# Performance work log

Hardware: AMD Instinct MI355X
Metric: run time of the kernel (lower is better)

Reference implementation:

```python
import jax, jax.numpy as jnp
import numpy as np

B, S, H = 2, 2048, 4096
NH, HD = 32, 128          # num attention heads, head dim (kv_channels)
KVH = 2                   # multi_query_group_num (KV heads)
ROT = HD // 2             # 64 rotary dims -> rope cache last-2 dim = 32
QKV = NH * HD + 2 * KVH * HD  # 4608


def apply_rope(x, rope):
    # x: [b, nh, s, hd]; rope: [b, s, ROT//2, 2]
    b, nh, s, hd = x.shape
    x_rot, x_pass = x[..., :ROT], x[..., ROT:]
    xs = x_rot.reshape(b, nh, s, ROT // 2, 2)
    rc = rope[:, :s].reshape(b, 1, s, ROT // 2, 2)
    out = jnp.stack([
        xs[..., 0] * rc[..., 0] - xs[..., 1] * rc[..., 1],
        xs[..., 1] * rc[..., 0] + xs[..., 0] * rc[..., 1],
    ], axis=-1).reshape(b, nh, s, ROT)
    return jnp.concatenate([out, x_pass], axis=-1)


def setup_inputs() -> dict:
    key = jax.random.key(0)
    ks = jax.random.split(key, 6)
    hidden_states = jax.random.normal(ks[0], (B, S, H), dtype=jnp.float32)
    rotary_pos_emb = jax.random.normal(ks[1], (B, S, ROT // 2, 2), dtype=jnp.float32)
    # causal mask: True = masked (strict upper triangle), matching module's ~tril
    causal = jnp.triu(jnp.ones((S, S), dtype=jnp.bool_), k=1)
    attention_mask = jnp.broadcast_to(causal[None, None], (B, 1, S, S))
    W_qkv = jax.random.normal(ks[2], (QKV, H), dtype=jnp.float32) * (1.0 / np.sqrt(H))
    b_qkv = jax.random.normal(ks[3], (QKV,), dtype=jnp.float32) * 0.02
    W_dense = jax.random.normal(ks[4], (H, NH * HD), dtype=jnp.float32) * (1.0 / np.sqrt(NH * HD))
    return {"hidden_states": hidden_states, "rotary_pos_emb": rotary_pos_emb,
            "attention_mask": attention_mask, "W_qkv": W_qkv, "b_qkv": b_qkv,
            "W_dense": W_dense}


def reference(hidden_states, rotary_pos_emb, attention_mask, W_qkv, b_qkv, W_dense):
    b, s, _ = hidden_states.shape
    mixed = hidden_states @ W_qkv.T + b_qkv  # [b, s, QKV]
    q, k, v = jnp.split(mixed, [NH * HD, NH * HD + KVH * HD], axis=-1)
    q = q.reshape(b, s, NH, HD).transpose(0, 2, 1, 3)   # [b, NH, s, hd]
    k = k.reshape(b, s, KVH, HD).transpose(0, 2, 1, 3)  # [b, KVH, s, hd]
    v = v.reshape(b, s, KVH, HD).transpose(0, 2, 1, 3)
    q = apply_rope(q, rotary_pos_emb)
    k = apply_rope(k, rotary_pos_emb)
    # GQA expand KV heads to NH
    rep = NH // KVH
    k = jnp.repeat(k, rep, axis=1)
    v = jnp.repeat(v, rep, axis=1)
    scale = 1.0 / np.sqrt(HD)
    scores = jnp.einsum('bhqd,bhkd->bhqk', q, k).astype(jnp.float32) * scale
    scores = jnp.where(attention_mask, -jnp.inf, scores)
    probs = jax.nn.softmax(scores, axis=-1).astype(v.dtype)
    ctx = jnp.einsum('bhqk,bhkd->bhqd', probs, v)       # [b, NH, s, hd]
    ctx = ctx.transpose(0, 2, 1, 3).reshape(b, s, NH * HD)
    return ctx @ W_dense.T
```

## Files before the change

kernel.cpp:

```cpp
#include <hip/hip_runtime.h>
#include <hip/hip_bf16.h>
#include <stdint.h>

#define Bb 2
#define Ss 2048
#define Hh 4096
#define NHh 32
#define HDd 128
#define KVHh 2

typedef __attribute__((ext_vector_type(8))) short bf16x8;
typedef __attribute__((ext_vector_type(4))) float f32x4;
typedef __attribute__((ext_vector_type(16))) float f32x16;
typedef __attribute__((ext_vector_type(4))) unsigned int u32x4;
typedef unsigned short u16;
typedef unsigned int u32;
typedef unsigned long long u64;

__device__ __forceinline__ u16 f2b(float f) {
  union { float f; u32 u; } v; v.f = f;
  u32 r = v.u + 0x7fffu + ((v.u >> 16) & 1u);
  return (u16)(r >> 16);
}
__device__ __forceinline__ float b2f(u16 h) {
  union { u32 u; float f; } v; v.u = ((u32)h) << 16;
  return v.f;
}

__device__ __forceinline__ u32 cvtpk(float lo, float hi_) {
  u32 r;
  asm("v_cvt_pk_bf16_f32 %0, %1, %2" : "=v"(r) : "v"(lo), "v"(hi_));
  return r;
}
__device__ __forceinline__ void plswap(u32& x, u32& y) {
  asm volatile("v_permlane32_swap_b32 %0, %1" : "+v"(x), "+v"(y));
}

__device__ __forceinline__ void gload_lds16(const u16* g, u16* l) {
  __builtin_amdgcn_global_load_lds(
      (const __attribute__((address_space(1))) u32*)(uintptr_t)g,
      (__attribute__((address_space(3))) u32*)(u32)(uintptr_t)l,
      16, 0, 0);
}

__global__ void cvt2_k(const float* __restrict__ a, u16* __restrict__ oa,
                       const float* __restrict__ b, u16* __restrict__ ob) {
  int i = blockIdx.x * blockDim.x + threadIdx.x;
  const float* src;
  u16* dst;
  int off;
  if (i < 4194304) { src = a; dst = oa; off = i; }
  else { src = b; dst = ob; off = i - 4194304; }
  int idx = off * 4;
  float4 v = *(const float4*)&src[idx];
  u64 pack = (u64)f2b(v.x) | ((u64)f2b(v.y) << 16) |
             ((u64)f2b(v.z) << 32) | ((u64)f2b(v.w) << 48);
  *(u64*)&dst[idx] = pack;
}

__global__ void cvtW_k(const float* __restrict__ in, u16* __restrict__ out) {
  int i = blockIdx.x * blockDim.x + threadIdx.x;
  int idx = i * 4;
  float4 v = *(const float4*)&in[idx];
  u64 pack = (u64)f2b(v.x) | ((u64)f2b(v.y) << 16) |
             ((u64)f2b(v.z) << 32) | ((u64)f2b(v.w) << 48);
  *(u64*)&out[idx] = pack;
}

__global__ void rope_k(u16* __restrict__ X, const float* __restrict__ rope, int nheads) {
  int i = blockIdx.x * blockDim.x + threadIdx.x;
  int p = i & 31;
  int s = (i >> 5) & (Ss - 1);
  int bh = i >> 16;
  if (bh >= Bb * nheads) return;
  int b = bh / nheads;
  size_t base = ((size_t)bh * Ss + s) * HDd + p * 2;
  u32 x01 = *(u32*)&X[base];
  float x0 = b2f((u16)(x01 & 0xffff));
  float x1 = b2f((u16)(x01 >> 16));
  float2 rc = *(const float2*)&rope[(((size_t)b * Ss + s) * 32 + p) * 2];
  float o0 = x0 * rc.x - x1 * rc.y;
  float o1 = x1 * rc.x + x0 * rc.y;
  u32 o = (u32)f2b(o0) | ((u32)f2b(o1) << 16);
  *(u32*)&X[base] = o;
}

template <int KK>
__device__ __forceinline__ void stage_tileA(const u16* __restrict__ gbase, u16* dst, int tid) {
#pragma unroll
  for (int li = 0; li < 2; ++li) {
    int t16 = li * 512 + tid;
    int rt = t16 >> 2, ct = t16 & 3;
    int cg = ct ^ ((rt >> 1) & 3);
    gload_lds16(gbase + (size_t)rt * KK + cg * 8, dst + t16 * 8);
  }
}
template <int KK>
__device__ __forceinline__ void stage_tileB(const u16* __restrict__ gbase, u16* dst, int tid) {
  int t16 = tid;
  int rt = t16 >> 2, ct = t16 & 3;
  int cg = ct ^ ((rt >> 1) & 3);
  gload_lds16(gbase + (size_t)rt * KK + cg * 8, dst + t16 * 8);
}

__device__ __forceinline__ bf16x8 frag128(const u16* buf, int row, int lk) {
  int ch = lk ^ ((row >> 1) & 3);
  return *(const bf16x8*)&buf[row * 32 + ch * 8];
}

template <int NN, int KK, int COLG>
__global__ __launch_bounds__(512, 4) void gemm_qkv(
    const u16* __restrict__ A, const u16* __restrict__ Bm,
    const float* __restrict__ bias,
    u16* __restrict__ Qb, u16* __restrict__ Kb, u16* __restrict__ Vb) {
  __shared__ u16 As[2][8192];
  __shared__ u16 Bs[2][4096];
  const int tid = threadIdx.x;
  const int wave = tid >> 6;
  const int lane = tid & 63;
  const int lr = lane & 15;
  const int lk = lane >> 4;
  const int wr = wave >> 1;
  const int wc = wave & 1;
  const int bid = blockIdx.x;
  const int xcd = bid & 7;
  const int local = bid >> 3;
  const int rlr = local / COLG;
  const int rlc = local - rlr * COLG;
  const int m0 = ((xcd >> 2) * 8 + rlr) * 256;
  const int n0 = ((xcd & 3) * COLG + rlc) * 128;
  const int NT = KK / 32;

  f32x4 acc[4][4];
#pragma unroll
  for (int i = 0; i < 4; ++i)
#pragma unroll
    for (int j = 0; j < 4; ++j) acc[i][j] = (f32x4){0.f, 0.f, 0.f, 0.f};

  const u16* Ab = A + (size_t)m0 * KK;
  const u16* Bw = Bm + (size_t)n0 * KK;

  stage_tileA<KK>(Ab, &As[0][0], tid);
  stage_tileB<KK>(Bw, &Bs[0][0], tid);
  asm volatile("s_waitcnt vmcnt(0)");
  __syncthreads();

  int cur = 0;
  for (int t = 0; t < NT; ++t) {
    if (t + 1 < NT) {
      stage_tileA<KK>(Ab + (t + 1) * 32, &As[cur ^ 1][0], tid);
      stage_tileB<KK>(Bw + (t + 1) * 32, &Bs[cur ^ 1][0], tid);
      asm volatile("s_waitcnt vmcnt(3)");
    } else {
      asm volatile("s_waitcnt vmcnt(0)");
    }
    __builtin_amdgcn_s_barrier();
    __builtin_amdgcn_sched_barrier(0);

    bf16x8 af[4], bf[4];
#pragma unroll
    for (int mi = 0; mi < 4; ++mi)
      af[mi] = frag128(&As[cur][0], wr * 64 + mi * 16 + lr, lk);
#pragma unroll
    for (int ni = 0; ni < 4; ++ni)
      bf[ni] = frag128(&Bs[cur][0], wc * 64 + ni * 16 + lr, lk);
    asm volatile("s_waitcnt lgkmcnt(0)");
    __builtin_amdgcn_sched_barrier(0);
    __builtin_amdgcn_s_setprio(1);
#pragma unroll
    for (int mi = 0; mi < 4; ++mi)
#pragma unroll
      for (int ni = 0; ni < 4; ++ni)
        acc[mi][ni] = __builtin_amdgcn_mfma_f32_16x16x32_bf16(af[mi], bf[ni], acc[mi][ni], 0, 0, 0);
    __builtin_amdgcn_s_setprio(0);
    __builtin_amdgcn_s_barrier();
    cur ^= 1;
  }

#pragma unroll
  for (int ni = 0; ni < 4; ++ni) {
    int n = n0 + wc * 64 + ni * 16 + lr;
    float bv = bias[n];
#pragma unroll
    for (int mi = 0; mi < 4; ++mi) {
      int mb = m0 + wr * 64 + mi * 16 + lk * 4;
#pragma unroll
      for (int j = 0; j < 4; ++j) {
        int m = mb + j;
        int bb = m >> 11;
        int ss = m & 2047;
        u16 hv = f2b(acc[mi][ni][j] + bv);
        if (n < 4096) {
          Qb[(((size_t)bb * NHh + (n >> 7)) * Ss + ss) * HDd + (n & 127)] = hv;
        } else if (n < 4352) {
          int idx2 = n - 4096;
          Kb[(((size_t)bb * KVHh + (idx2 >> 7)) * Ss + ss) * HDd + (idx2 & 127)] = hv;
        } else {
          int idx2 = n - 4352;
          Vb[(((size_t)bb * KVHh + (idx2 >> 7)) * Ss + ss) * HDd + (idx2 & 127)] = hv;
        }
      }
    }
  }
}

__global__ __launch_bounds__(512, 2) void gemm_dense8p(
    const u16* __restrict__ A, const u16* __restrict__ Bm,
    float* __restrict__ Cout) {
  __shared__ u16 Ar[3][256 * 64];
  __shared__ u16 Bd[2][128 * 64];
  const int tid = threadIdx.x;
  const int wave = tid >> 6;
  const int lane = tid & 63;
  const int lr = lane & 15;
  const int lk = lane >> 4;
  const int wr = wave >> 1;
  const int wc = wave & 1;
  const int bid = blockIdx.x;
  const int xcd = bid & 7;
  const int local = bid >> 3;
  const int m0 = ((xcd >> 2) * 8 + (local >> 3)) * 256;
  const int n0 = ((xcd & 3) * 8 + (local & 7)) * 128;

  f32x4 acc[4][4];
#pragma unroll
  for (int i = 0; i < 4; ++i)
#pragma unroll
    for (int j = 0; j < 4; ++j) acc[i][j] = (f32x4){0.f, 0.f, 0.f, 0.f};

  auto STAGE_A = [&](int j, int ring) {
    if (j >= 64) return;
#pragma unroll
    for (int li = 0; li < 4; ++li) {
      int t16 = li * 512 + tid;
      int row = t16 >> 3, c = t16 & 7;
      int cs = c ^ (row & 7);
      gload_lds16(A + (size_t)(m0 + row) * 4096 + j * 64 + cs * 8,
                  &Ar[ring][0] + t16 * 8);
    }
  };
  auto STAGE_B = [&](int j) {
    if (j >= 64) return;
#pragma unroll
    for (int li = 0; li < 2; ++li) {
      int t16 = li * 512 + tid;
      int row = t16 >> 3, c = t16 & 7;
      int cs = c ^ (row & 7);
      gload_lds16(Bm + (size_t)(n0 + row) * 4096 + j * 64 + cs * 8,
                  &Bd[j & 1][0] + t16 * 8);
    }
  };

  STAGE_A(0, 0); STAGE_B(0);
  STAGE_A(1, 1); STAGE_B(1);
  asm volatile("s_waitcnt vmcnt(6)");
  __builtin_amdgcn_s_barrier();
  __builtin_amdgcn_sched_barrier(0);

  int ra = 0;
  int ra2 = 2;
  for (int kt = 0; kt < 64; ++kt) {
    const u16* Acur = &Ar[ra][0];
    const u16* Bt = &Bd[kt & 1][0];
    auto rdA = [&](int r, int kk) {
      int ch = (kk * 4 + lk) ^ (r & 7);
      return *(const bf16x8*)&Acur[r * 64 + ch * 8];
    };
    auto rdB = [&](int r, int kk) {
      int ch = (kk * 4 + lk) ^ (r & 7);
      return *(const bf16x8*)&Bt[r * 64 + ch * 8];
    };

    bf16x8 bfr[4][2], af[2][2];
#pragma unroll
    for (int ni = 0; ni < 4; ++ni)
#pragma unroll
      for (int kk = 0; kk < 2; ++kk)
        bfr[ni][kk] = rdB(wc * 64 + ni * 16 + lr, kk);
#pragma unroll
    for (int i = 0; i < 2; ++i)
#pragma unroll
      for (int kk = 0; kk < 2; ++kk)
        af[i][kk] = rdA(wr * 64 + i * 16 + lr, kk);
    STAGE_A(kt + 2, ra2);
    __builtin_amdgcn_s_barrier();
    asm volatile("s_waitcnt lgkmcnt(0)");
    __builtin_amdgcn_sched_barrier(0);
    __builtin_amdgcn_s_setprio(1);
#pragma unroll
    for (int i = 0; i < 2; ++i)
#pragma unroll
      for (int ni = 0; ni < 4; ++ni)
#pragma unroll
        for (int kk = 0; kk < 2; ++kk)
          acc[i][ni] = __builtin_amdgcn_mfma_f32_16x16x32_bf16(af[i][kk], bfr[ni][kk], acc[i][ni], 0, 0, 0);
    __builtin_amdgcn_s_setprio(0);
    __builtin_amdgcn_s_barrier();

#pragma unroll
    for (int i = 0; i < 2; ++i)
#pragma unroll
      for (int kk = 0; kk < 2; ++kk)
        af[i][kk] = rdA(wr * 64 + (2 + i) * 16 + lr, kk);
    STAGE_B(kt + 2);
    __builtin_amdgcn_s_barrier();
    asm volatile("s_waitcnt lgkmcnt(0)");
    __builtin_amdgcn_sched_barrier(0);
    __builtin_amdgcn_s_setprio(1);
#pragma unroll
    for (int i = 0; i < 2; ++i)
#pragma unroll
      for (int ni = 0; ni < 4; ++ni)
#pragma unroll
        for (int kk = 0; kk < 2; ++kk)
          acc[2 + i][ni] = __builtin_amdgcn_mfma_f32_16x16x32_bf16(af[i][kk], bfr[ni][kk], acc[2 + i][ni], 0, 0, 0);
    __builtin_amdgcn_s_setprio(0);
    if (kt < 62) {
      asm volatile("s_waitcnt vmcnt(6)");
    } else {
      asm volatile("s_waitcnt vmcnt(0)");
    }
    __builtin_amdgcn_s_barrier();
    __builtin_amdgcn_sched_barrier(0);

    ra = (ra == 2) ? 0 : ra + 1;
    ra2 = (ra2 == 2) ? 0 : ra2 + 1;
  }

#pragma unroll
  for (int mi = 0; mi < 4; ++mi)
#pragma unroll
    for (int ni = 0; ni < 4; ++ni) {
      int col = n0 + wc * 64 + ni * 16 + lr;
      int rowb = m0 + wr * 64 + mi * 16 + lk * 4;
#pragma unroll
      for (int j = 0; j < 4; ++j)
        Cout[(size_t)(rowb + j) * 4096 + col] = acc[mi][ni][j];
    }
}

__global__ __launch_bounds__(512, 2) void attn_k(
    const u16* __restrict__ Qb, const u16* __restrict__ Kb,
    const u16* __restrict__ Vb, const float* __restrict__ rope,
    u16* __restrict__ Ctx) {
  __shared__ u16 Kt[2][64 * 128];
  __shared__ u16 Vt[2][128 * 64];
  const int tid = threadIdx.x;
  const int w = tid >> 6;
  const int lane = tid & 63;
  const int l31 = lane & 31;
  const int hi = lane >> 5;
  const int h = blockIdx.y, b = blockIdx.z;
  const int hkv = h >> 4;
  const u16* Qp = Qb + ((size_t)(b * NHh + h)) * Ss * HDd;
  const u16* Kp = Kb + ((size_t)(b * KVHh + hkv)) * Ss * HDd;
  const u16* Vp = Vb + ((size_t)(b * KVHh + hkv)) * Ss * HDd;

  const float scale = 0.08838834764831845f;
  const float L2E = 1.4426950408889634f;

  for (int hp = 0; hp < 2; ++hp) {
    const int qt = hp == 0 ? (7 - (int)blockIdx.x) : (int)blockIdx.x;
    const int qs = qt * 256;
    const int qw = qs + w * 32;
    const int qrow = qw + l31;
    const int nt = qs / 64 + 4;

    bf16x8 qf[8];
#pragma unroll
    for (int ds = 0; ds < 8; ++ds)
      qf[ds] = *(const bf16x8*)&Qp[(size_t)qrow * HDd + ds * 16 + hi * 8];
#pragma unroll
    for (int ds = 0; ds < 4; ++ds) {
      bf16x8 q = qf[ds];
      bf16x8 o;
#pragma unroll
      for (int i = 0; i < 4; ++i) {
        int p = ds * 8 + hi * 4 + i;
        float2 rc = *(const float2*)&rope[(((size_t)b * Ss + qrow) * 32 + p) * 2];
        float x0 = b2f((u16)q[2 * i]), x1 = b2f((u16)q[2 * i + 1]);
        o[2 * i] = (short)f2b(x0 * rc.x - x1 * rc.y);
        o[2 * i + 1] = (short)f2b(x1 * rc.x + x0 * rc.y);
      }
      qf[ds] = o;
    }

    f32x16 accO[4];
#pragma unroll
    for (int i = 0; i < 4; ++i)
#pragma unroll
      for (int r = 0; r < 16; ++r) accO[i][r] = 0.f;
    float m_r = -3.0e38f, l_r = 0.f;

    {
#pragma unroll
      for (int i = 0; i < 2; ++i) {
        int slot = w * 2 + i;
        int r = slot * 4 + (lane >> 4);
        int p = lane & 15;
        int gc = (p & 8) | ((p ^ r) & 7);
        gload_lds16(Kp + (size_t)r * HDd + gc * 8, &Kt[0][slot * 512]);
      }
      bf16x8 v0 = *(const bf16x8*)&Vp[(size_t)lane * HDd + w * 16];
      bf16x8 v1 = *(const bf16x8*)&Vp[(size_t)lane * HDd + w * 16 + 8];
      u32x4 sv = __builtin_bit_cast(u32x4, (lane & 1) ? v0 : v1);
      u32x4 rv;
      rv.x = __shfl_xor(sv.x, 1); rv.y = __shfl_xor(sv.y, 1);
      rv.z = __shfl_xor(sv.z, 1); rv.w = __shfl_xor(sv.w, 1);
      bf16x8 recv = __builtin_bit_cast(bf16x8, rv);
      int kvp = lane >> 1;
#pragma unroll
      for (int i = 0; i < 8; ++i) {
        int d = w * 16 + (lane & 1) * 8 + i;
        u16 lo = (lane & 1) ? (u16)recv[i] : (u16)v0[i];
        u16 hb = (lane & 1) ? (u16)v1[i] : (u16)recv[i];
        u32 val = (u32)lo | ((u32)hb << 16);
        int cp = (kvp >> 2) ^ (d & 7);
        *(u32*)&Vt[0][d * 64 + cp * 8 + (kvp & 3) * 2] = val;
      }
    }
    __syncthreads();

    for (int t = 0; t < nt; ++t) {
      const int j0 = t * 64;
      const int cur = t & 1;
      const bool havenext = (t + 1 < nt);
      bf16x8 nv0, nv1;
      if (havenext) {
        const int j1 = j0 + 64;
#pragma unroll
        for (int i = 0; i < 2; ++i) {
          int slot = w * 2 + i;
          int r = slot * 4 + (lane >> 4);
          int p = lane & 15;
          int gc = (p & 8) | ((p ^ r) & 7);
          gload_lds16(Kp + (size_t)(j1 + r) * HDd + gc * 8, &Kt[cur ^ 1][slot * 512]);
        }
        nv0 = *(const bf16x8*)&Vp[(size_t)(j1 + lane) * HDd + w * 16];
        nv1 = *(const bf16x8*)&Vp[(size_t)(j1 + lane) * HDd + w * 16 + 8];
      }

      if (j0 <= qw + 31) {
        f32x16 aS[2];
#pragma unroll
        for (int a = 0; a < 2; ++a)
#pragma unroll
          for (int r = 0; r < 16; ++r) aS[a][r] = 0.f;
#pragma unroll
        for (int kvb = 0; kvb < 2; ++kvb) {
          int r = kvb * 32 + l31;
#pragma unroll
          for (int ds = 0; ds < 8; ++ds) {
            int c = ds * 2 + hi;
            int cp = (c & 8) | ((c ^ r) & 7);
            bf16x8 kf = *(const bf16x8*)&Kt[cur][r * 128 + cp * 8];
            aS[kvb] = __builtin_amdgcn_mfma_f32_32x32x16_bf16(kf, qf[ds], aS[kvb], 0, 0, 0);
          }
        }
        const bool needmask = (j0 + 63 > qw);
        float mx = -3.0e38f;
#pragma unroll
        for (int a = 0; a < 2; ++a)
#pragma unroll
          for (int r = 0; r < 16; ++r) {
            float s = aS[a][r] * scale;
            if (needmask) {
              int kv = j0 + a * 32 + (r & 3) + 8 * (r >> 2) + 4 * hi;
              s = (kv > qrow) ? -3.0e38f : s;
            }
            aS[a][r] = s;
            mx = fmaxf(mx, s);
          }
        mx = fmaxf(mx, __shfl_xor(mx, 32));
        if (!__all(mx - m_r <= 8.0f)) {
          float mnew = fmaxf(m_r, mx);
          float corr = __builtin_amdgcn_exp2f((m_r - mnew) * L2E);
          l_r *= corr;
#pragma unroll
          for (int i = 0; i < 4; ++i)
#pragma unroll
            for (int r = 0; r < 16; ++r) accO[i][r] *= corr;
          m_r = mnew;
        }
        float sum = 0.f;
#pragma unroll
        for (int a = 0; a < 2; ++a)
#pragma unroll
          for (int r = 0; r < 16; ++r) {
            float pe = __builtin_amdgcn_exp2f((aS[a][r] - m_r) * L2E);
            aS[a][r] = pe;
            sum += pe;
          }
        sum += __shfl_xor(sum, 32);
        l_r += sum;

        u32 cc0[2][4], cc1[2][4];
#pragma unroll
        for (int a = 0; a < 2; ++a)
#pragma unroll
          for (int g = 0; g < 4; ++g) {
            cc0[a][g] = cvtpk(aS[a][g * 4 + 0], aS[a][g * 4 + 1]);
            cc1[a][g] = cvtpk(aS[a][g * 4 + 2], aS[a][g * 4 + 3]);
          }
        bf16x8 pa[4];
#pragma unroll
        for (int ks = 0; ks < 4; ++ks) {
          int a = ks >> 1, g0 = (ks & 1) * 2;
          u32 w0 = cc0[a][g0], w2 = cc0[a][g0 + 1];
          u32 w1 = cc1[a][g0], w3 = cc1[a][g0 + 1];
          plswap(w0, w2);
          plswap(w1, w3);
          u32x4 tv; tv.x = w0; tv.y = w1; tv.z = w2; tv.w = w3;
          pa[ks] = __builtin_bit_cast(bf16x8, tv);
        }
#pragma unroll
        for (int dblk = 0; dblk < 4; ++dblk) {
          int d = dblk * 32 + l31;
#pragma unroll
          for (int ks = 0; ks < 4; ++ks) {
            int c = ks * 2 + hi;
            int cp = c ^ (d & 7);
            bf16x8 vf = *(const bf16x8*)&Vt[cur][d * 64 + cp * 8];
            accO[dblk] = __builtin_amdgcn_mfma_f32_32x32x16_bf16(vf, pa[ks], accO[dblk], 0, 0, 0);
          }
        }
      }

      if (havenext) {
        u32x4 sv = __builtin_bit_cast(u32x4, (lane & 1) ? nv0 : nv1);
        u32x4 rv;
        rv.x = __shfl_xor(sv.x, 1); rv.y = __shfl_xor(sv.y, 1);
        rv.z = __shfl_xor(sv.z, 1); rv.w = __shfl_xor(sv.w, 1);
        bf16x8 recv = __builtin_bit_cast(bf16x8, rv);
        int kvp = lane >> 1;
#pragma unroll
        for (int i = 0; i < 8; ++i) {
          int d = w * 16 + (lane & 1) * 8 + i;
          u16 lo = (lane & 1) ? (u16)recv[i] : (u16)nv0[i];
          u16 hb = (lane & 1) ? (u16)nv1[i] : (u16)recv[i];
          u32 val = (u32)lo | ((u32)hb << 16);
          int cp = (kvp >> 2) ^ (d & 7);
          *(u32*)&Vt[cur ^ 1][d * 64 + cp * 8 + (kvp & 3) * 2] = val;
        }
      }
      __syncthreads();
    }

    {
      float il = 1.0f / l_r;
      size_t rb = ((size_t)b * Ss + qrow) * (size_t)(NHh * HDd) + (size_t)h * HDd;
#pragma unroll
      for (int dblk = 0; dblk < 4; ++dblk)
#pragma unroll
        for (int g = 0; g < 4; ++g) {
          int d0 = dblk * 32 + g * 8 + hi * 4;
          u64 pack = (u64)f2b(accO[dblk][g * 4 + 0] * il) |
                     ((u64)f2b(accO[dblk][g * 4 + 1] * il) << 16) |
                     ((u64)f2b(accO[dblk][g * 4 + 2] * il) << 32) |
                     ((u64)f2b(accO[dblk][g * 4 + 3] * il) << 48);
          *(u64*)&Ctx[rb + d0] = pack;
        }
    }
    __syncthreads();
  }
}

extern "C" void kernel_launch(void* const* d_in, const int* in_sizes, int n_in,
                              void* d_out, int out_size, void* d_ws, size_t ws_size,
                              hipStream_t stream) {
  const float* hidden = (const float*)d_in[0];
  const float* rope = (const float*)d_in[1];
  const float* Wqkv = (const float*)d_in[3];
  const float* bqkv = (const float*)d_in[4];
  const float* Wdense = (const float*)d_in[5];
  float* out = (float*)d_out;

  char* w = (char*)d_ws;
  u16* Xbf = (u16*)w;
  u16* ctx = Xbf;
  w += (size_t)33554432;
  u16* Wq = (u16*)w;
  u16* Wd = Wq;
  w += (size_t)37748736;
  u16* Qb = (u16*)w; w += (size_t)33554432;
  u16* Kb = (u16*)w; w += (size_t)2097152;
  u16* Vb = (u16*)w; w += (size_t)2097152;

  cvt2_k<<<34816, 256, 0, stream>>>(hidden, Xbf, Wqkv, Wq);
  gemm_qkv<4608, 4096, 9><<<dim3(576), 512, 0, stream>>>(
      Xbf, Wq, bqkv, Qb, Kb, Vb);
  rope_k<<<(Bb * KVHh * Ss * 32 + 255) / 256, 256, 0, stream>>>(Kb, rope, KVHh);
  cvtW_k<<<16384, 256, 0, stream>>>(Wdense, Wd);
  attn_k<<<dim3(4, NHh, Bb), 512, 0, stream>>>(Qb, Kb, Vb, rope, ctx);
  gemm_dense8p<<<dim3(512), 512, 0, stream>>>(ctx, Wd, out);
}
```

Before: 483.2 us.

## Enlarge dense GEMM tile to 256x256 with half-split double-buffered staging

Replaces the 256x128 dense output-projection GEMM with a 256x256 tile per block (256 blocks instead of 512). Waves are rearranged 2x4, each computing 128x64. A and B are staged in 128-row halves into a two-stage shared-memory buffer, with loads interleaved across four MFMA phases per k-step. The goal is higher arithmetic intensity and less global and LDS traffic per FLOP. The cost is more accumulator registers, which may hurt occupancy under launch_bounds(512,2), and 256 blocks only fill the 256 CUs once.

New measurement: 471.6 us, median of 3. -2.4%, faster.

```diff
diff --git a/kernel.cpp b/kernel.cpp
--- a/kernel.cpp
+++ b/kernel.cpp
@@ -204,71 +204,68 @@
   }
 }
 
-__global__ __launch_bounds__(512, 2) void gemm_dense8p(
+__global__ __launch_bounds__(512, 2) void gemm_d256(
     const u16* __restrict__ A, const u16* __restrict__ Bm,
     float* __restrict__ Cout) {
-  __shared__ u16 Ar[3][256 * 64];
-  __shared__ u16 Bd[2][128 * 64];
+  __shared__ u16 SM[2][4][8192];
   const int tid = threadIdx.x;
   const int wave = tid >> 6;
   const int lane = tid & 63;
   const int lr = lane & 15;
   const int lk = lane >> 4;
-  const int wr = wave >> 1;
-  const int wc = wave & 1;
+  const int wr = wave >> 2;
+  const int wc = wave & 3;
   const int bid = blockIdx.x;
   const int xcd = bid & 7;
   const int local = bid >> 3;
-  const int m0 = ((xcd >> 2) * 8 + (local >> 3)) * 256;
-  const int n0 = ((xcd & 3) * 8 + (local & 7)) * 128;
-
-  f32x4 acc[4][4];
-#pragma unroll
-  for (int i = 0; i < 4; ++i)
+  const int m0 = ((xcd >> 2) * 8 + (local >> 2)) * 256;
+  const int n0 = ((xcd & 3) * 4 + (local & 3)) * 256;
+  const int NT = 64;
+
+  f32x4 acc[8][4];
+#pragma unroll
+  for (int i = 0; i < 8; ++i)
 #pragma unroll
     for (int j = 0; j < 4; ++j) acc[i][j] = (f32x4){0.f, 0.f, 0.f, 0.f};
 
-  auto STAGE_A = [&](int j, int ring) {
-    if (j >= 64) return;
-#pragma unroll
-    for (int li = 0; li < 4; ++li) {
-      int t16 = li * 512 + tid;
-      int row = t16 >> 3, c = t16 & 7;
-      int cs = c ^ (row & 7);
-      gload_lds16(A + (size_t)(m0 + row) * 4096 + j * 64 + cs * 8,
-                  &Ar[ring][0] + t16 * 8);
-    }
-  };
-  auto STAGE_B = [&](int j) {
-    if (j >= 64) return;
+  auto stage_half = [&](const u16* grows, int j, u16* dst) {
+    if (j >= NT) return;
 #pragma unroll
     for (int li = 0; li < 2; ++li) {
       int t16 = li * 512 + tid;
       int row = t16 >> 3, c = t16 & 7;
       int cs = c ^ (row & 7);
-      gload_lds16(Bm + (size_t)(n0 + row) * 4096 + j * 64 + cs * 8,
-                  &Bd[j & 1][0] + t16 * 8);
+      gload_lds16(grows + (size_t)row * 4096 + j * 64 + cs * 8, dst + t16 * 8);
     }
   };
-
-  STAGE_A(0, 0); STAGE_B(0);
-  STAGE_A(1, 1); STAGE_B(1);
-  asm volatile("s_waitcnt vmcnt(6)");
+  const u16* Ah0g = A + (size_t)m0 * 4096;
+  const u16* Ah1g = A + (size_t)(m0 + 128) * 4096;
+  const u16* Bh0g = Bm + (size_t)n0 * 4096;
+  const u16* Bh1g = Bm + (size_t)(n0 + 128) * 4096;
+
+  stage_half(Ah0g, 0, &SM[0][2][0]);
+  stage_half(Ah1g, 0, &SM[0][3][0]);
+  stage_half(Bh0g, 0, &SM[0][0][0]);
+  stage_half(Bh1g, 0, &SM[0][1][0]);
+  stage_half(Bh0g, 1, &SM[1][0][0]);
+  stage_half(Bh1g, 1, &SM[1][1][0]);
+  asm volatile("s_waitcnt vmcnt(0)");
   __builtin_amdgcn_s_barrier();
   __builtin_amdgcn_sched_barrier(0);
 
-  int ra = 0;
-  int ra2 = 2;
-  for (int kt = 0; kt < 64; ++kt) {
-    const u16* Acur = &Ar[ra][0];
-    const u16* Bt = &Bd[kt & 1][0];
+  for (int kt = 0; kt < NT; ++kt) {
+    const int cur = kt & 1;
+    const int nxt = cur ^ 1;
+    const u16* Ahl = &SM[cur][2 + wr][0];
+    const u16* Bhl = &SM[cur][wc >> 1][0];
+    const int rB0 = (wc & 1) * 64;
     auto rdA = [&](int r, int kk) {
       int ch = (kk * 4 + lk) ^ (r & 7);
-      return *(const bf16x8*)&Acur[r * 64 + ch * 8];
+      return *(const bf16x8*)&Ahl[r * 64 + ch * 8];
     };
     auto rdB = [&](int r, int kk) {
       int ch = (kk * 4 + lk) ^ (r & 7);
-      return *(const bf16x8*)&Bt[r * 64 + ch * 8];
+      return *(const bf16x8*)&Bhl[r * 64 + ch * 8];
     };
 
     bf16x8 bfr[4][2], af[2][2];
@@ -276,13 +273,13 @@
     for (int ni = 0; ni < 4; ++ni)
 #pragma unroll
       for (int kk = 0; kk < 2; ++kk)
-        bfr[ni][kk] = rdB(wc * 64 + ni * 16 + lr, kk);
+        bfr[ni][kk] = rdB(rB0 + ni * 16 + lr, kk);
 #pragma unroll
     for (int i = 0; i < 2; ++i)
 #pragma unroll
       for (int kk = 0; kk < 2; ++kk)
-        af[i][kk] = rdA(wr * 64 + i * 16 + lr, kk);
-    STAGE_A(kt + 2, ra2);
+        af[i][kk] = rdA(i * 16 + lr, kk);
+    stage_half(Ah0g, kt + 1, &SM[nxt][2][0]);
     __builtin_amdgcn_s_barrier();
     asm volatile("s_waitcnt lgkmcnt(0)");
     __builtin_amdgcn_sched_barrier(0);
@@ -301,8 +298,8 @@
     for (int i = 0; i < 2; ++i)
 #pragma unroll
       for (int kk = 0; kk < 2; ++kk)
-        af[i][kk] = rdA(wr * 64 + (2 + i) * 16 + lr, kk);
-    STAGE_B(kt + 2);
+        af[i][kk] = rdA((2 + i) * 16 + lr, kk);
+    stage_half(Ah1g, kt + 1, &SM[nxt][3][0]);
     __builtin_amdgcn_s_barrier();
     asm volatile("s_waitcnt lgkmcnt(0)");
     __builtin_amdgcn_sched_barrier(0);
@@ -315,24 +312,61 @@
         for (int kk = 0; kk < 2; ++kk)
           acc[2 + i][ni] = __builtin_amdgcn_mfma_f32_16x16x32_bf16(af[i][kk], bfr[ni][kk], acc[2 + i][ni], 0, 0, 0);
     __builtin_amdgcn_s_setprio(0);
-    if (kt < 62) {
-      asm volatile("s_waitcnt vmcnt(6)");
+    __builtin_amdgcn_s_barrier();
+
+#pragma unroll
+    for (int i = 0; i < 2; ++i)
+#pragma unroll
+      for (int kk = 0; kk < 2; ++kk)
+        af[i][kk] = rdA((4 + i) * 16 + lr, kk);
+    stage_half(Bh0g, kt + 2, &SM[cur][0][0]);
+    __builtin_amdgcn_s_barrier();
+    asm volatile("s_waitcnt lgkmcnt(0)");
+    __builtin_amdgcn_sched_barrier(0);
+    __builtin_amdgcn_s_setprio(1);
+#pragma unroll
+    for (int i = 0; i < 2; ++i)
+#pragma unroll
+      for (int ni = 0; ni < 4; ++ni)
+#pragma unroll
+        for (int kk = 0; kk < 2; ++kk)
+          acc[4 + i][ni] = __builtin_amdgcn_mfma_f32_16x16x32_bf16(af[i][kk], bfr[ni][kk], acc[4 + i][ni], 0, 0, 0);
+    __builtin_amdgcn_s_setprio(0);
+    __builtin_amdgcn_s_barrier();
+
+#pragma unroll
+    for (int i = 0; i < 2; ++i)
+#pragma unroll
+      for (int kk = 0; kk < 2; ++kk)
+        af[i][kk] = rdA((6 + i) * 16 + lr, kk);
+    stage_half(Bh1g, kt + 2, &SM[cur][1][0]);
+    __builtin_amdgcn_s_barrier();
+    asm volatile("s_waitcnt lgkmcnt(0)");
+    __builtin_amdgcn_sched_barrier(0);
+    __builtin_amdgcn_s_setprio(1);
+#pragma unroll
+    for (int i = 0; i < 2; ++i)
+#pragma unroll
+      for (int ni = 0; ni < 4; ++ni)
+#pragma unroll
+        for (int kk = 0; kk < 2; ++kk)
+          acc[6 + i][ni] = __builtin_amdgcn_mfma_f32_16x16x32_bf16(af[i][kk], bfr[ni][kk], acc[6 + i][ni], 0, 0, 0);
+    __builtin_amdgcn_s_setprio(0);
+    if (kt < NT - 2) {
+      asm volatile("s_waitcnt vmcnt(4)");
     } else {
       asm volatile("s_waitcnt vmcnt(0)");
     }
     __builtin_amdgcn_s_barrier();
     __builtin_amdgcn_sched_barrier(0);
-
-    ra = (ra == 2) ? 0 : ra + 1;
-    ra2 = (ra2 == 2) ? 0 : ra2 + 1;
   }
 
 #pragma unroll
-  for (int mi = 0; mi < 4; ++mi)
+  for (int mi = 0; mi < 8; ++mi)
 #pragma unroll
     for (int ni = 0; ni < 4; ++ni) {
       int col = n0 + wc * 64 + ni * 16 + lr;
-      int rowb = m0 + wr * 64 + mi * 16 + lk * 4;
+      int rowb = m0 + wr * 128 + mi * 16 + lk * 4;
 #pragma unroll
       for (int j = 0; j < 4; ++j)
         Cout[(size_t)(rowb + j) * 4096 + col] = acc[mi][ni][j];
@@ -592,5 +626,5 @@
   rope_k<<<(Bb * KVHh * Ss * 32 + 255) / 256, 256, 0, stream>>>(Kb, rope, KVHh);
   cvtW_k<<<16384, 256, 0, stream>>>(Wdense, Wd);
   attn_k<<<dim3(4, NHh, Bb), 512, 0, stream>>>(Qb, Kb, Vb, rope, ctx);
-  gemm_dense8p<<<dim3(512), 512, 0, stream>>>(ctx, Wd, out);
-}
+  gemm_d256<<<dim3(256), 512, 0, stream>>>(ctx, Wd, out);
+}
```
